# Kernel tuning notes

Measured on AMD Instinct MI355X. Metric: run time of the kernel, lower is better.

Reference implementation:

```python
import jax, jax.numpy as jnp
import numpy as np

B, N1, N2, D, H, DFF = 128, 256, 256, 256, 8, 1024
DH = D // H


def _ln(x, g, b, eps=1e-6):
    mu = jnp.mean(x, axis=-1, keepdims=True)
    var = jnp.mean(jnp.square(x - mu), axis=-1, keepdims=True)
    return g * (x - mu) / jnp.sqrt(var + eps) + b


def setup_inputs() -> dict:
    key = jax.random.key(0)
    ks = jax.random.split(key, 16)
    x1 = jax.random.normal(ks[0], (B, N1, D), jnp.float32)
    x2 = jax.random.normal(ks[1], (B, N2, D), jnp.float32)
    adj1 = (jax.random.uniform(ks[2], (B, N1, N1)) < 0.1).astype(jnp.float32)
    adj1 = jnp.maximum(adj1, jnp.eye(N1, dtype=jnp.float32)[None])
    mask1 = jnp.ones((B, N1), jnp.float32)
    mask2 = jnp.ones((B, N2), jnp.float32)
    s = 0.02
    Wq = jax.random.normal(ks[3], (D, D), jnp.float32) * s
    Wk = jax.random.normal(ks[4], (D, D), jnp.float32) * s
    Wv = jax.random.normal(ks[5], (D, D), jnp.float32) * s
    Wo = jax.random.normal(ks[6], (D, D), jnp.float32) * s
    W1 = jax.random.normal(ks[7], (D, DFF), jnp.float32) * s
    W2 = jax.random.normal(ks[8], (DFF, D), jnp.float32) * s
    return {
        "x1": x1, "adj1": adj1, "mask1": mask1, "x2": x2, "mask2": mask2,
        "Wq": Wq, "bq": jnp.zeros((D,), jnp.float32),
        "Wk": Wk, "bk": jnp.zeros((D,), jnp.float32),
        "Wv": Wv, "bv": jnp.zeros((D,), jnp.float32),
        "Wo": Wo, "bo": jnp.zeros((D,), jnp.float32),
        "W1": W1, "b1": jnp.zeros((DFF,), jnp.float32),
        "W2": W2, "b2": jnp.zeros((D,), jnp.float32),
        "g1": jnp.ones((D,), jnp.float32), "be1": jnp.zeros((D,), jnp.float32),
        "g2": jnp.ones((D,), jnp.float32), "be2": jnp.zeros((D,), jnp.float32),
    }


def reference(x1, adj1, mask1, x2, mask2, Wq, bq, Wk, bk, Wv, bv, Wo, bo,
              W1, b1, W2, b2, g1, be1, g2, be2):
    # Multi-head graph attention: self-attention on x1 masked by adjacency,
    # plus cross-attention from x1 to x2 masked by mask2 (PrismGATLayer).
    q = (x1 @ Wq + bq).reshape(B, N1, H, DH)
    k1 = (x1 @ Wk + bk).reshape(B, N1, H, DH)
    v1 = (x1 @ Wv + bv).reshape(B, N1, H, DH)
    k2 = (x2 @ Wk + bk).reshape(B, N2, H, DH)
    v2 = (x2 @ Wv + bv).reshape(B, N2, H, DH)
    scale = 1.0 / jnp.sqrt(jnp.float32(DH))

    s1 = jnp.einsum('bqhd,bkhd->bhqk', q, k1) * scale            # [B,H,N1,N1]
    m1 = adj1[:, None, :, :] * mask1[:, None, None, :]
    s1 = jnp.where(m1 > 0, s1, jnp.float32(-1e9))
    c1 = jnp.einsum('bhqk,bkhd->bqhd', jax.nn.softmax(s1, axis=-1), v1)

    s2 = jnp.einsum('bqhd,bkhd->bhqk', q, k2) * scale            # [B,H,N1,N2]
    s2 = jnp.where(mask2[:, None, None, :] > 0, s2, jnp.float32(-1e9))
    c2 = jnp.einsum('bhqk,bkhd->bqhd', jax.nn.softmax(s2, axis=-1), v2)

    attn = (c1 + c2).reshape(B, N1, D) @ Wo + bo
    out1 = _ln(x1 + attn, g1, be1)                               # dropout = identity (eval)
    ffn = jax.nn.relu(out1 @ W1 + b1) @ W2 + b2
    return _ln(out1 + ffn, g2, be2)
```

## Files before the change

kernel.cpp:

```cpp
#include <hip/hip_runtime.h>
#include <hip/hip_bf16.h>
#include <stdint.h>

#define B_   128
#define N1_  256
#define N2_  256
#define D_   256
#define H_   8
#define DH_  32
#define DFF_ 1024
#define M_   (B_*N1_)

typedef unsigned short ushortT;
typedef unsigned int   uintT;
typedef short bf16x8 __attribute__((ext_vector_type(8)));
typedef float f32x4  __attribute__((ext_vector_type(4)));

#if __has_builtin(__builtin_amdgcn_exp2f)
#define EXP2(x) __builtin_amdgcn_exp2f(x)
#else
#define EXP2(x) exp2f(x)
#endif

__device__ __forceinline__ float b2f(ushortT u){ return __uint_as_float(((uintT)u)<<16); }
__device__ __forceinline__ ushortT f2b(float f){
  uintT u = __float_as_uint(f);
  uintT r = (u + 0x7fffu + ((u>>16)&1u)) >> 16;
  return (ushortT)r;
}

__device__ __forceinline__ int sniff_wave(const ushortT* x){
  const int e = (x[threadIdx.x & 63] >> 7) & 0xff;
  const unsigned long long bad = __ballot(e < 100 || e > 135);
  return __popcll(bad) >= 12;
}
__device__ __forceinline__ float ldin(const void* p, size_t i, int f32){
  return f32 ? ((const float*)p)[i] : b2f(((const ushortT*)p)[i]);
}

__global__ __launch_bounds__(256) void conv_bf16_kernel(
    const void* __restrict__ X, ushortT* __restrict__ Y, int n8,
    const ushortT* __restrict__ sniffp)
{
  const int in_f32 = sniff_wave(sniffp);
  int i = blockIdx.x * 256 + threadIdx.x;
  if (i >= n8) return;
  size_t base = (size_t)i * 8;
  if (in_f32) {
    float4 a = *(const float4*)((const float*)X + base);
    float4 b = *(const float4*)((const float*)X + base + 4);
    ushort4 o0, o1;
    o0.x=f2b(a.x); o0.y=f2b(a.y); o0.z=f2b(a.z); o0.w=f2b(a.w);
    o1.x=f2b(b.x); o1.y=f2b(b.y); o1.z=f2b(b.z); o1.w=f2b(b.w);
    *(ushort4*)(Y + base)     = o0;
    *(ushort4*)(Y + base + 4) = o1;
  } else {
    *(uint4*)(Y + base) = *(const uint4*)((const ushortT*)X + base);
  }
}

__global__ __launch_bounds__(256) void transpose_w_kernel(
    const void* __restrict__ W, ushortT* __restrict__ Wt, int K, int N,
    const ushortT* __restrict__ sniffp)
{
  const int in_f32 = sniff_wave(sniffp);
  __shared__ float t[32][33];
  const int tx = threadIdx.x & 31, ty = threadIdx.x >> 5;
  const int n0 = blockIdx.x * 32, k0 = blockIdx.y * 32;
  #pragma unroll
  for (int i = 0; i < 4; i++)
    t[ty + 8*i][tx] = ldin(W, (size_t)(k0 + ty + 8*i) * N + n0 + tx, in_f32);
  __syncthreads();
  #pragma unroll
  for (int i = 0; i < 4; i++)
    Wt[(size_t)(n0 + ty + 8*i) * K + k0 + tx] = f2b(t[tx][ty + 8*i]);
}

__global__ __launch_bounds__(256) void pack_adj_kernel(
    const void* __restrict__ ADJ, uintT* __restrict__ AB,
    const ushortT* __restrict__ sniffp)
{
  const int in_f32 = sniff_wave(sniffp);
  const int idx = blockIdx.x * 256 + threadIdx.x;
  const size_t base = (size_t)(idx >> 3) * 256 + (size_t)(idx & 7) * 32;
  uintT bits = 0;
  if (in_f32) {
    const float* ap = (const float*)ADJ + base;
    #pragma unroll
    for (int j4 = 0; j4 < 8; j4++) {
      float4 v = *(const float4*)(ap + j4 * 4);
      bits |= (v.x > 0.f ? 1u : 0u) << (j4 * 4 + 0);
      bits |= (v.y > 0.f ? 1u : 0u) << (j4 * 4 + 1);
      bits |= (v.z > 0.f ? 1u : 0u) << (j4 * 4 + 2);
      bits |= (v.w > 0.f ? 1u : 0u) << (j4 * 4 + 3);
    }
  } else {
    const ushortT* ap = (const ushortT*)ADJ + base;
    #pragma unroll
    for (int j = 0; j < 32; j++)
      bits |= (b2f(ap[j]) > 0.f ? 1u : 0u) << j;
  }
  AB[idx] = bits;
}

__global__ __launch_bounds__(256) void pack_mask_kernel(
    const void* __restrict__ M1, const void* __restrict__ M2,
    uintT* __restrict__ MW, const ushortT* __restrict__ sniffp)
{
  const int in_f32 = sniff_wave(sniffp);
  const int idx = blockIdx.x * 256 + threadIdx.x;
  const int src = idx >> 10;
  const void* MP = src ? M2 : M1;
  const size_t base = (size_t)((idx >> 3) & 127) * 256 + (size_t)(idx & 7) * 32;
  uintT bits = 0;
  #pragma unroll
  for (int j = 0; j < 32; j++)
    bits |= (ldin(MP, base + j, in_f32) > 0.f ? 1u : 0u) << j;
  MW[idx] = bits;
}

__global__ __launch_bounds__(256) void gemm128_kernel(
    const ushortT* __restrict__ A, const ushortT* __restrict__ Bt,
    const void* __restrict__ bias, ushortT* __restrict__ C,
    int M, int N, int K, int relu, float alpha,
    const ushortT* __restrict__ sniffp)
{
  __shared__ ushortT Al[128 * 40];
  __shared__ ushortT Bl[128 * 40];

  const int tid = threadIdx.x;
  const int in_f32 = sniff_wave(sniffp);
  const int wave = tid >> 6, lane = tid & 63;
  const int l15 = lane & 15, l4 = lane >> 4;
  const int wm = wave & 1, wn = wave >> 1;

  const int lin = blockIdx.x + gridDim.x * blockIdx.y;
  const int chunk = (gridDim.x * gridDim.y) >> 3;
  const int gsw = (lin & 7) * chunk + (lin >> 3);
  const int ylog = 31 - __clz(gridDim.y);
  const int bx = gsw >> ylog, by = gsw & (gridDim.y - 1);
  const int row0 = bx * 128, col0 = by * 128;
  const int m0 = wm * 64, n0 = wn * 64;

  f32x4 acc[4][4];
  #pragma unroll
  for (int i = 0; i < 4; i++)
    #pragma unroll
    for (int j = 0; j < 4; j++) acc[i][j] = (f32x4)0.f;

  const int sr = tid >> 2;
  const int sk = (tid & 3) * 8;

  const ushortT* Ap = &A[(size_t)(row0 + sr) * K + sk];
  const ushortT* Bp = &Bt[(size_t)(col0 + sr) * K + sk];
  const size_t step64 = (size_t)64 * K;

  uint4 a0 = *(const uint4*)Ap;
  uint4 a1 = *(const uint4*)(Ap + step64);
  uint4 b0 = *(const uint4*)Bp;
  uint4 b1 = *(const uint4*)(Bp + step64);

  for (int kt = 0; kt < K; kt += 32) {
    __syncthreads();
    *(uint4*)&Al[sr * 40 + sk]        = a0;
    *(uint4*)&Al[(sr + 64) * 40 + sk] = a1;
    *(uint4*)&Bl[sr * 40 + sk]        = b0;
    *(uint4*)&Bl[(sr + 64) * 40 + sk] = b1;
    __syncthreads();
    if (kt + 32 < K) {
      a0 = *(const uint4*)(Ap + kt + 32);
      a1 = *(const uint4*)(Ap + step64 + kt + 32);
      b0 = *(const uint4*)(Bp + kt + 32);
      b1 = *(const uint4*)(Bp + step64 + kt + 32);
    }
    bf16x8 af[4], bf[4];
    #pragma unroll
    for (int mt = 0; mt < 4; mt++)
      af[mt] = *(const bf16x8*)&Al[(m0 + mt * 16 + l15) * 40 + l4 * 8];
    #pragma unroll
    for (int nt = 0; nt < 4; nt++)
      bf[nt] = *(const bf16x8*)&Bl[(n0 + nt * 16 + l15) * 40 + l4 * 8];
    #pragma unroll
    for (int mt = 0; mt < 4; mt++)
      #pragma unroll
      for (int nt = 0; nt < 4; nt++)
        acc[mt][nt] = __builtin_amdgcn_mfma_f32_16x16x32_bf16(af[mt], bf[nt], acc[mt][nt], 0, 0, 0);
  }

  #pragma unroll
  for (int nt = 0; nt < 4; nt++) {
    int col = col0 + n0 + nt * 16 + l15;
    float bb = ldin(bias, col, in_f32);
    #pragma unroll
    for (int mt = 0; mt < 4; mt++) {
      #pragma unroll
      for (int r = 0; r < 4; r++) {
        float v = (acc[mt][nt][r] + bb) * alpha;
        if (relu) v = fmaxf(v, 0.f);
        int row = row0 + m0 + mt * 16 + l4 * 4 + r;
        C[(size_t)row * N + col] = f2b(v);
      }
    }
  }
}

__global__ __launch_bounds__(256) void gemm_qkv_kernel(
    const ushortT* __restrict__ A, const ushortT* __restrict__ Bt,
    const void* __restrict__ b0p, const void* __restrict__ b1p,
    const void* __restrict__ b2p,
    ushortT* __restrict__ C0, ushortT* __restrict__ C1,
    ushortT* __restrict__ C2,
    int K, float alpha2, const ushortT* __restrict__ sniffp)
{
  __shared__ ushortT Al[128 * 40];
  __shared__ ushortT Bl[128 * 40];

  const int tid = threadIdx.x;
  const int in_f32 = sniff_wave(sniffp);
  const int wave = tid >> 6, lane = tid & 63;
  const int l15 = lane & 15, l4 = lane >> 4;
  const int wm = wave & 1, wn = wave >> 1;

  const int gy = gridDim.y;
  const int lin = blockIdx.x + gridDim.x * blockIdx.y;
  const int chunk = (gridDim.x * gy) >> 3;
  const int gsw = (lin & 7) * chunk + (lin >> 3);
  const int bx = gsw / gy, by = gsw - bx * gy;
  const int row0 = bx * 128, col0 = by * 128;
  const int m0 = wm * 64, n0 = wn * 64;

  f32x4 acc[4][4];
  #pragma unroll
  for (int i = 0; i < 4; i++)
    #pragma unroll
    for (int j = 0; j < 4; j++) acc[i][j] = (f32x4)0.f;

  const int sr = tid >> 2;
  const int sk = (tid & 3) * 8;

  const ushortT* Ap = &A[(size_t)(row0 + sr) * K + sk];
  const ushortT* Bp = &Bt[(size_t)(col0 + sr) * K + sk];
  const size_t step64 = (size_t)64 * K;

  uint4 a0 = *(const uint4*)Ap;
  uint4 a1 = *(const uint4*)(Ap + step64);
  uint4 b0 = *(const uint4*)Bp;
  uint4 b1 = *(const uint4*)(Bp + step64);

  for (int kt = 0; kt < K; kt += 32) {
    __syncthreads();
    *(uint4*)&Al[sr * 40 + sk]        = a0;
    *(uint4*)&Al[(sr + 64) * 40 + sk] = a1;
    *(uint4*)&Bl[sr * 40 + sk]        = b0;
    *(uint4*)&Bl[(sr + 64) * 40 + sk] = b1;
    __syncthreads();
    if (kt + 32 < K) {
      a0 = *(const uint4*)(Ap + kt + 32);
      a1 = *(const uint4*)(Ap + step64 + kt + 32);
      b0 = *(const uint4*)(Bp + kt + 32);
      b1 = *(const uint4*)(Bp + step64 + kt + 32);
    }
    bf16x8 af[4], bf[4];
    #pragma unroll
    for (int mt = 0; mt < 4; mt++)
      af[mt] = *(const bf16x8*)&Al[(m0 + mt * 16 + l15) * 40 + l4 * 8];
    #pragma unroll
    for (int nt = 0; nt < 4; nt++)
      bf[nt] = *(const bf16x8*)&Bl[(n0 + nt * 16 + l15) * 40 + l4 * 8];
    #pragma unroll
    for (int mt = 0; mt < 4; mt++)
      #pragma unroll
      for (int nt = 0; nt < 4; nt++)
        acc[mt][nt] = __builtin_amdgcn_mfma_f32_16x16x32_bf16(af[mt], bf[nt], acc[mt][nt], 0, 0, 0);
  }

  const int seg = col0 >> 8;
  const int cb  = col0 & 255;

  if (seg == 1) {
    const int bb  = row0 >> 8;
    const int tl0 = (row0 & 255) + m0 + l4 * 4;
    #pragma unroll
    for (int nt = 0; nt < 4; nt++) {
      const int col = cb + n0 + nt * 16 + l15;
      const float bbv = ldin(b1p, col, in_f32);
      #pragma unroll
      for (int mt = 0; mt < 4; mt++) {
        ushort4 o;
        o.x = f2b(acc[mt][nt][0] + bbv);
        o.y = f2b(acc[mt][nt][1] + bbv);
        o.z = f2b(acc[mt][nt][2] + bbv);
        o.w = f2b(acc[mt][nt][3] + bbv);
        *(ushort4*)&C1[(size_t)bb * 65536 + (size_t)col * 256 + tl0 + mt * 16] = o;
      }
    }
  } else {
    ushortT* C = seg ? C2 : C0;
    const void* bp = seg ? b2p : b0p;
    const float al = seg ? alpha2 : 1.f;
    #pragma unroll
    for (int nt = 0; nt < 4; nt++) {
      const int col = cb + n0 + nt * 16 + l15;
      const float bb = ldin(bp, col, in_f32);
      #pragma unroll
      for (int mt = 0; mt < 4; mt++) {
        #pragma unroll
        for (int r = 0; r < 4; r++) {
          const float v = (acc[mt][nt][r] + bb) * al;
          const int row = row0 + m0 + mt * 16 + l4 * 4 + r;
          C[(size_t)row * 256 + col] = f2b(v);
        }
      }
    }
  }
}

#define LNROWS 4
__global__ __launch_bounds__(256) void add_ln_kernel(
    const void* __restrict__ X, const ushortT* __restrict__ Y,
    const void* __restrict__ gamma, const void* __restrict__ beta,
    void* __restrict__ out, const ushortT* __restrict__ sniffp,
    int x_dyn, int store_dyn)
{
  const int in_f32 = sniff_wave(sniffp);
  const int xf32 = x_dyn ? in_f32 : 0;
  const int lane = threadIdx.x & 63;
  const int gw = blockIdx.x * 4 + (threadIdx.x >> 6);
  const int d0 = lane * 4;

  float g[4], be[4];
  if (in_f32) {
    float4 gv = *(const float4*)((const float*)gamma + d0);
    float4 bv = *(const float4*)((const float*)beta  + d0);
    g[0]=gv.x; g[1]=gv.y; g[2]=gv.z; g[3]=gv.w;
    be[0]=bv.x; be[1]=bv.y; be[2]=bv.z; be[3]=bv.w;
  } else {
    ushort4 gv = *(const ushort4*)((const ushortT*)gamma + d0);
    ushort4 bv = *(const ushort4*)((const ushortT*)beta  + d0);
    g[0]=b2f(gv.x); g[1]=b2f(gv.y); g[2]=b2f(gv.z); g[3]=b2f(gv.w);
    be[0]=b2f(bv.x); be[1]=b2f(bv.y); be[2]=b2f(bv.z); be[3]=b2f(bv.w);
  }

  const int row0 = gw * LNROWS;

  float v[LNROWS][4];
  #pragma unroll
  for (int rr = 0; rr < LNROWS; rr++) {
    const size_t base = (size_t)(row0 + rr) * D_ + d0;
    const ushort4 yv = *(const ushort4*)(Y + base);
    if (xf32) {
      float4 xv = *(const float4*)((const float*)X + base);
      v[rr][0] = xv.x + b2f(yv.x); v[rr][1] = xv.y + b2f(yv.y);
      v[rr][2] = xv.z + b2f(yv.z); v[rr][3] = xv.w + b2f(yv.w);
    } else {
      ushort4 xv = *(const ushort4*)((const ushortT*)X + base);
      v[rr][0] = b2f(xv.x) + b2f(yv.x); v[rr][1] = b2f(xv.y) + b2f(yv.y);
      v[rr][2] = b2f(xv.z) + b2f(yv.z); v[rr][3] = b2f(xv.w) + b2f(yv.w);
    }
  }

  #pragma unroll
  for (int rr = 0; rr < LNROWS; rr++) {
    float s = (v[rr][0] + v[rr][1]) + (v[rr][2] + v[rr][3]);
    float q = (v[rr][0]*v[rr][0] + v[rr][1]*v[rr][1])
            + (v[rr][2]*v[rr][2] + v[rr][3]*v[rr][3]);
    #pragma unroll
    for (int off = 1; off < 64; off <<= 1) {
      s += __shfl_xor(s, off, 64);
      q += __shfl_xor(q, off, 64);
    }
    const float mu   = s * (1.f / D_);
    const float var  = q * (1.f / D_) - mu * mu;
    const float rstd = rsqrtf(var + 1e-6f);
    const size_t base = (size_t)(row0 + rr) * D_ + d0;
    if (store_dyn && in_f32) {
      float4 o;
      o.x = g[0]*(v[rr][0]-mu)*rstd + be[0];
      o.y = g[1]*(v[rr][1]-mu)*rstd + be[1];
      o.z = g[2]*(v[rr][2]-mu)*rstd + be[2];
      o.w = g[3]*(v[rr][3]-mu)*rstd + be[3];
      *(float4*)((float*)out + base) = o;
    } else {
      ushort4 o;
      o.x = f2b(g[0]*(v[rr][0]-mu)*rstd + be[0]);
      o.y = f2b(g[1]*(v[rr][1]-mu)*rstd + be[1]);
      o.z = f2b(g[2]*(v[rr][2]-mu)*rstd + be[2]);
      o.w = f2b(g[3]*(v[rr][3]-mu)*rstd + be[3]);
      *(ushort4*)((ushortT*)out + base) = o;
    }
  }
}

__global__ __launch_bounds__(256, 4) void attn_mfma_kernel(
    ushortT* __restrict__ QC,
    const ushortT* __restrict__ K1, const ushortT* __restrict__ K2,
    const ushortT* __restrict__ V1t, const ushortT* __restrict__ V2t,
    const uintT* __restrict__ AB, const uintT* __restrict__ MW)
{
  const int lin = blockIdx.x + (blockIdx.y << 2) + (blockIdx.z << 5);
  const int gsw = (lin & 7) * 512 + (lin >> 3);
  const int b = gsw >> 5, h = (gsw >> 2) & 7, qt = gsw & 3;
  const int q0 = qt * 64;
  const int tid = threadIdx.x;
  const int wave = tid >> 6, lane = tid & 63;
  const int l15 = lane & 15, l4 = lane >> 4;

  __shared__ __align__(16) ushortT P[64][256];

  const size_t bh = (size_t)b * 256;
  const int prow = wave * 16 + l15;
  const uintT swz = (uintT)((prow & 7) << 4);
  char* Prow = (char*)&P[prow][0];

  uintT adjr[8];
  {
    const uintT* abp = AB + ((size_t)(b * 256 + q0 + prow)) * 8;
    const uint4 a0 = *(const uint4*)abp;
    const uint4 a1 = *(const uint4*)(abp + 4);
    adjr[0]=a0.x; adjr[1]=a0.y; adjr[2]=a0.z; adjr[3]=a0.w;
    adjr[4]=a1.x; adjr[5]=a1.y; adjr[6]=a1.z; adjr[7]=a1.w;
  }

  const bf16x8 af = *(const bf16x8*)&QC[(bh + q0 + wave*16 + l15) * 256 + h*32 + l4*8];

  f32x4 acc0 = (f32x4)0.f, acc1 = (f32x4)0.f;

  #pragma unroll 1
  for (int src = 0; src < 2; src++) {
    const ushortT* Kp  = src ? K2  : K1;
    const ushortT* Vtp = src ? V2t : V1t;

    const uintT* mwp = MW + (src * 128 + b) * 8;
    uintT mww[8];
    #pragma unroll
    for (int w = 0; w < 8; w++) mww[w] = mwp[w];

    float rsum = 0.f;
    #pragma unroll
    for (int c = 0; c < 4; c++) {
      bf16x8 kf[4];
      #pragma unroll
      for (int j = 0; j < 4; j++)
        kf[j] = *(const bf16x8*)&Kp[(bh + (c*4 + j)*16 + l15) * 256 + h*32 + l4*8];
      #pragma unroll
      for (int j = 0; j < 4; j++) {
        const int nt = c*4 + j;
        const f32x4 s4 = __builtin_amdgcn_mfma_f32_16x16x32_bf16(kf[j], af, (f32x4)0.f, 0, 0, 0);
        const int tb = nt*16 + l4*4;
        const int sh = tb & 31;
        uintT bits = mww[nt >> 1] >> sh;
        if (src == 0) bits &= adjr[nt >> 1] >> sh;
        const float e0 = (bits & 1u) ? EXP2(s4[0]) : 0.f;
        const float e1 = (bits & 2u) ? EXP2(s4[1]) : 0.f;
        const float e2 = (bits & 4u) ? EXP2(s4[2]) : 0.f;
        const float e3 = (bits & 8u) ? EXP2(s4[3]) : 0.f;
        rsum += (e0 + e1) + (e2 + e3);
        uintT pk01, pk23;
        asm("v_cvt_pk_bf16_f32 %0, %1, %2" : "=v"(pk01) : "v"(e0), "v"(e1));
        asm("v_cvt_pk_bf16_f32 %0, %1, %2" : "=v"(pk23) : "v"(e2), "v"(e3));
        uint2 pw; pw.x = pk01; pw.y = pk23;
        *(uint2*)(Prow + (((uintT)(tb*2)) ^ swz)) = pw;
      }
    }
    rsum += __shfl_xor(rsum, 16, 64);
    rsum += __shfl_xor(rsum, 32, 64);
    const float rv = 1.f / rsum;
    float rvr[4];
    #pragma unroll
    for (int r = 0; r < 4; r++) rvr[r] = __shfl(rv, l4*4 + r, 64);

    f32x4 o0 = (f32x4)0.f, o1 = (f32x4)0.f;
    __builtin_amdgcn_s_setprio(1);
    #pragma unroll
    for (int kt = 0; kt < 8; kt++) {
      const bf16x8 ap = *(const bf16x8*)(Prow + (((uintT)(kt*64 + l4*16)) ^ swz));
      const bf16x8 v0 = *(const bf16x8*)&Vtp[(bh + h*32 + l15) * 256 + kt*32 + l4*8];
      const bf16x8 v1 = *(const bf16x8*)&Vtp[(bh + h*32 + 16 + l15) * 256 + kt*32 + l4*8];
      o0 = __builtin_amdgcn_mfma_f32_16x16x32_bf16(ap, v0, o0, 0, 0, 0);
      o1 = __builtin_amdgcn_mfma_f32_16x16x32_bf16(ap, v1, o1, 0, 0, 0);
    }
    __builtin_amdgcn_s_setprio(0);
    #pragma unroll
    for (int r = 0; r < 4; r++) { acc0[r] += o0[r] * rvr[r]; acc1[r] += o1[r] * rvr[r]; }
  }

  #pragma unroll
  for (int r = 0; r < 4; r++) {
    const int row = (int)(bh + q0 + wave*16 + l4*4 + r);
    QC[(size_t)row * 256 + h*32 + l15]      = f2b(acc0[r]);
    QC[(size_t)row * 256 + h*32 + 16 + l15] = f2b(acc1[r]);
  }
}

extern "C" void kernel_launch(void* const* d_in, const int* in_sizes, int n_in,
                              void* d_out, int out_size, void* d_ws, size_t ws_size,
                              hipStream_t stream) {
  const void* x1    = d_in[0];
  const void* adj1  = d_in[1];
  const void* mask1 = d_in[2];
  const void* x2    = d_in[3];
  const void* mask2 = d_in[4];
  const void* Wq = d_in[5];  const void* bq = d_in[6];
  const void* Wk = d_in[7];  const void* bk = d_in[8];
  const void* Wv = d_in[9];  const void* bv = d_in[10];
  const void* Wo = d_in[11]; const void* bo = d_in[12];
  const void* W1 = d_in[13]; const void* b1 = d_in[14];
  const void* W2 = d_in[15]; const void* b2 = d_in[16];
  const void* g1 = d_in[17]; const void* be1= d_in[18];
  const void* g2 = d_in[19]; const void* be2= d_in[20];
  const ushortT* sniffp = (const ushortT*)x1;

  ushortT* ws = (ushortT*)d_ws;
  const size_t SZ = (size_t)M_ * D_;
  ushortT* S0 = ws;
  ushortT* S1 = ws + SZ;
  ushortT* S2 = ws + 2*SZ;
  ushortT* S3 = ws + 3*SZ;
  ushortT* S4 = ws + 4*SZ;
  ushortT* S5 = ws + 5*SZ;
  ushortT* dOut = (ushortT*)d_out;

  ushortT* Wkt = S5;
  ushortT* Wvt = S5 + 65536;
  ushortT* Wqt = S5 + 131072;
  ushortT* Wot = S2;
  ushortT* W1t = dOut;
  ushortT* W2t = dOut + 262144;
  ushortT* qbuf = dOut + 524288;
  uintT* AB = (uintT*)(dOut + 9437184);
  uintT* MWp = AB + 262144;

  const float qalpha = 0.25503486f;

  dim3 blk(256);
  dim3 gGemmD(M_/128, D_/128);
  dim3 gGemmF(M_/128, DFF_/128);
  dim3 gQKV(M_/128, 6);
  dim3 gKV(M_/128, 4);
  dim3 gT256(8, 8);
  const int n8 = (int)(SZ / 8);

  pack_adj_kernel<<<dim3(1024), blk, 0, stream>>>(adj1, AB, sniffp);
  pack_mask_kernel<<<dim3(8), blk, 0, stream>>>(mask1, mask2, MWp, sniffp);

  conv_bf16_kernel<<<dim3((n8+255)/256), blk, 0, stream>>>(x2, S2, n8, sniffp);
  transpose_w_kernel<<<gT256, blk, 0, stream>>>(Wk, Wkt, D_, D_, sniffp);
  transpose_w_kernel<<<gT256, blk, 0, stream>>>(Wv, Wvt, D_, D_, sniffp);
  transpose_w_kernel<<<gT256, blk, 0, stream>>>(Wq, Wqt, D_, D_, sniffp);

  gemm_qkv_kernel<<<gKV, blk, 0, stream>>>(S2, S5, bk, bv, nullptr,
                                           S3, S1, nullptr, D_, 1.f, sniffp);

  conv_bf16_kernel<<<dim3((n8+255)/256), blk, 0, stream>>>(x1, S0, n8, sniffp);

  gemm_qkv_kernel<<<gQKV, blk, 0, stream>>>(S0, S5, bk, bv, bq,
                                            S2, S4, qbuf, D_, qalpha, sniffp);

  transpose_w_kernel<<<dim3(DFF_/32, D_/32), blk, 0, stream>>>(W1, W1t, D_, DFF_, sniffp);
  transpose_w_kernel<<<dim3(D_/32, DFF_/32), blk, 0, stream>>>(W2, W2t, DFF_, D_, sniffp);

  attn_mfma_kernel<<<dim3(N1_/64, H_, B_), blk, 0, stream>>>(
      qbuf, S2, S3, S4, S1, AB, MWp);

  transpose_w_kernel<<<gT256, blk, 0, stream>>>(Wo, Wot, D_, D_, sniffp);
  gemm128_kernel<<<gGemmD, blk, 0, stream>>>(qbuf, Wot, bo, S3, M_, D_, D_, 0, 1.f, sniffp);

  add_ln_kernel<<<dim3(M_/16), blk, 0, stream>>>(x1, S3, g1, be1, S0, sniffp, 1, 0);

  gemm128_kernel<<<gGemmF, blk, 0, stream>>>(S0, W1t, b1, S1, M_, DFF_, D_, 1, 1.f, sniffp);

  gemm128_kernel<<<gGemmD, blk, 0, stream>>>(S1, W2t, b2, S5, M_, D_, DFF_, 0, 1.f, sniffp);

  add_ln_kernel<<<dim3(M_/16), blk, 0, stream>>>(S0, S5, g2, be2, d_out, sniffp, 0, 1);
}
```

Baseline: 472.0 us.

## Load GEMM tiles directly into LDS with global_load_lds and XOR swizzle

Both GEMM kernels now load A/B tiles straight from global memory into shared memory using the global_load_lds builtin instead of staging through registers. The padded 40-element row stride is replaced by a 32-element stride with an XOR column swizzle on both write and read sides to avoid bank conflicts. This drops register staging and VGPR pressure, but it also removes the register prefetch of the next K tile, so global load latency is no longer overlapped with MFMA work within a block. The correctness of this relies on the load-to-LDS completing before the barrier.

```diff
diff --git a/kernel.cpp b/kernel.cpp
--- a/kernel.cpp
+++ b/kernel.cpp
@@ -21,6 +21,11 @@
 #else
 #define EXP2(x) exp2f(x)
 #endif
+
+#define GLOAD16(gsrc, ldst)                                                  \
+  __builtin_amdgcn_global_load_lds(                                          \
+      (const __attribute__((address_space(1))) unsigned int*)(gsrc),         \
+      (__attribute__((address_space(3))) unsigned int*)(ldst), 16, 0, 0)
 
 __device__ __forceinline__ float b2f(ushortT u){ return __uint_as_float(((uintT)u)<<16); }
 __device__ __forceinline__ ushortT f2b(float f){
@@ -125,8 +130,8 @@
     int M, int N, int K, int relu, float alpha,
     const ushortT* __restrict__ sniffp)
 {
-  __shared__ ushortT Al[128 * 40];
-  __shared__ ushortT Bl[128 * 40];
+  __shared__ ushortT Al[128 * 32];
+  __shared__ ushortT Bl[128 * 32];
 
   const int tid = threadIdx.x;
   const int in_f32 = sniff_wave(sniffp);
@@ -149,37 +154,31 @@
     for (int j = 0; j < 4; j++) acc[i][j] = (f32x4)0.f;
 
   const int sr = tid >> 2;
-  const int sk = (tid & 3) * 8;
-
-  const ushortT* Ap = &A[(size_t)(row0 + sr) * K + sk];
-  const ushortT* Bp = &Bt[(size_t)(col0 + sr) * K + sk];
+  const int csw = ((tid & 3) ^ ((sr >> 1) & 3)) * 8;
+  const int rsw = (l4 ^ ((l15 >> 1) & 3)) * 8;
+
+  const ushortT* Ap = &A[(size_t)(row0 + sr) * K + csw];
+  const ushortT* Bp = &Bt[(size_t)(col0 + sr) * K + csw];
   const size_t step64 = (size_t)64 * K;
-
-  uint4 a0 = *(const uint4*)Ap;
-  uint4 a1 = *(const uint4*)(Ap + step64);
-  uint4 b0 = *(const uint4*)Bp;
-  uint4 b1 = *(const uint4*)(Bp + step64);
+  ushortT* Ald0 = &Al[tid * 8];
+  ushortT* Ald1 = &Al[2048 + tid * 8];
+  ushortT* Bld0 = &Bl[tid * 8];
+  ushortT* Bld1 = &Bl[2048 + tid * 8];
 
   for (int kt = 0; kt < K; kt += 32) {
     __syncthreads();
-    *(uint4*)&Al[sr * 40 + sk]        = a0;
-    *(uint4*)&Al[(sr + 64) * 40 + sk] = a1;
-    *(uint4*)&Bl[sr * 40 + sk]        = b0;
-    *(uint4*)&Bl[(sr + 64) * 40 + sk] = b1;
+    GLOAD16(Ap + kt,          Ald0);
+    GLOAD16(Ap + step64 + kt, Ald1);
+    GLOAD16(Bp + kt,          Bld0);
+    GLOAD16(Bp + step64 + kt, Bld1);
     __syncthreads();
-    if (kt + 32 < K) {
-      a0 = *(const uint4*)(Ap + kt + 32);
-      a1 = *(const uint4*)(Ap + step64 + kt + 32);
-      b0 = *(const uint4*)(Bp + kt + 32);
-      b1 = *(const uint4*)(Bp + step64 + kt + 32);
-    }
     bf16x8 af[4], bf[4];
     #pragma unroll
     for (int mt = 0; mt < 4; mt++)
-      af[mt] = *(const bf16x8*)&Al[(m0 + mt * 16 + l15) * 40 + l4 * 8];
+      af[mt] = *(const bf16x8*)&Al[(m0 + mt * 16 + l15) * 32 + rsw];
     #pragma unroll
     for (int nt = 0; nt < 4; nt++)
-      bf[nt] = *(const bf16x8*)&Bl[(n0 + nt * 16 + l15) * 40 + l4 * 8];
+      bf[nt] = *(const bf16x8*)&Bl[(n0 + nt * 16 + l15) * 32 + rsw];
     #pragma unroll
     for (int mt = 0; mt < 4; mt++)
       #pragma unroll
@@ -212,8 +211,8 @@
     ushortT* __restrict__ C2,
     int K, float alpha2, const ushortT* __restrict__ sniffp)
 {
-  __shared__ ushortT Al[128 * 40];
-  __shared__ ushortT Bl[128 * 40];
+  __shared__ ushortT Al[128 * 32];
+  __shared__ ushortT Bl[128 * 32];
 
   const int tid = threadIdx.x;
   const int in_f32 = sniff_wave(sniffp);
@@ -236,37 +235,31 @@
     for (int j = 0; j < 4; j++) acc[i][j] = (f32x4)0.f;
 
   const int sr = tid >> 2;
-  const int sk = (tid & 3) * 8;
-
-  const ushortT* Ap = &A[(size_t)(row0 + sr) * K + sk];
-  const ushortT* Bp = &Bt[(size_t)(col0 + sr) * K + sk];
+  const int csw = ((tid & 3) ^ ((sr >> 1) & 3)) * 8;
+  const int rsw = (l4 ^ ((l15 >> 1) & 3)) * 8;
+
+  const ushortT* Ap = &A[(size_t)(row0 + sr) * K + csw];
+  const ushortT* Bp = &Bt[(size_t)(col0 + sr) * K + csw];
   const size_t step64 = (size_t)64 * K;
-
-  uint4 a0 = *(const uint4*)Ap;
-  uint4 a1 = *(const uint4*)(Ap + step64);
-  uint4 b0 = *(const uint4*)Bp;
-  uint4 b1 = *(const uint4*)(Bp + step64);
+  ushortT* Ald0 = &Al[tid * 8];
+  ushortT* Ald1 = &Al[2048 + tid * 8];
+  ushortT* Bld0 = &Bl[tid * 8];
+  ushortT* Bld1 = &Bl[2048 + tid * 8];
 
   for (int kt = 0; kt < K; kt += 32) {
     __syncthreads();
-    *(uint4*)&Al[sr * 40 + sk]        = a0;
-    *(uint4*)&Al[(sr + 64) * 40 + sk] = a1;
-    *(uint4*)&Bl[sr * 40 + sk]        = b0;
-    *(uint4*)&Bl[(sr + 64) * 40 + sk] = b1;
+    GLOAD16(Ap + kt,          Ald0);
+    GLOAD16(Ap + step64 + kt, Ald1);
+    GLOAD16(Bp + kt,          Bld0);
+    GLOAD16(Bp + step64 + kt, Bld1);
     __syncthreads();
-    if (kt + 32 < K) {
-      a0 = *(const uint4*)(Ap + kt + 32);
-      a1 = *(const uint4*)(Ap + step64 + kt + 32);
-      b0 = *(const uint4*)(Bp + kt + 32);
-      b1 = *(const uint4*)(Bp + step64 + kt + 32);
-    }
     bf16x8 af[4], bf[4];
     #pragma unroll
     for (int mt = 0; mt < 4; mt++)
-      af[mt] = *(const bf16x8*)&Al[(m0 + mt * 16 + l15) * 40 + l4 * 8];
+      af[mt] = *(const bf16x8*)&Al[(m0 + mt * 16 + l15) * 32 + rsw];
     #pragma unroll
     for (int nt = 0; nt < 4; nt++)
-      bf[nt] = *(const bf16x8*)&Bl[(n0 + nt * 16 + l15) * 40 + l4 * 8];
+      bf[nt] = *(const bf16x8*)&Bl[(n0 + nt * 16 + l15) * 32 + rsw];
     #pragma unroll
     for (int mt = 0; mt < 4; mt++)
       #pragma unroll
```

Result: no change. 479.5 us (+1.6%).

## Fuse input conversion into QKV GEMM and merge prep kernels into one launch

Applied to the files above, without the earlier changes.

Drops the separate x1/x2 fp32-to-bf16 conversion kernels; the merged K/V/Q projection GEMM now loads fp32 inputs directly and converts them in registers. The two QKV GEMM launches become one 10-column grid covering both x2 (K,V) and x1 (K,V,Q). All weight transposes and the adjacency and mask bit-packing move into a single prep kernel. This cuts launch count and the round trip of writing and re-reading the bf16 copies of the activations. The cost is more register and ALU work inside the GEMM loads, plus a wider grid.

```diff
diff --git a/kernel.cpp b/kernel.cpp
--- a/kernel.cpp
+++ b/kernel.cpp
@@ -38,35 +38,29 @@
   return f32 ? ((const float*)p)[i] : b2f(((const ushortT*)p)[i]);
 }
 
-__global__ __launch_bounds__(256) void conv_bf16_kernel(
-    const void* __restrict__ X, ushortT* __restrict__ Y, int n8,
-    const ushortT* __restrict__ sniffp)
-{
-  const int in_f32 = sniff_wave(sniffp);
-  int i = blockIdx.x * 256 + threadIdx.x;
-  if (i >= n8) return;
-  size_t base = (size_t)i * 8;
-  if (in_f32) {
-    float4 a = *(const float4*)((const float*)X + base);
-    float4 b = *(const float4*)((const float*)X + base + 4);
-    ushort4 o0, o1;
-    o0.x=f2b(a.x); o0.y=f2b(a.y); o0.z=f2b(a.z); o0.w=f2b(a.w);
-    o1.x=f2b(b.x); o1.y=f2b(b.y); o1.z=f2b(b.z); o1.w=f2b(b.w);
-    *(ushort4*)(Y + base)     = o0;
-    *(ushort4*)(Y + base + 4) = o1;
+template<int F32>
+__device__ __forceinline__ uint4 ldA8(const void* A, size_t e){
+  if (F32) {
+    const float* p = (const float*)A + e;
+    const float4 a = *(const float4*)p;
+    const float4 b = *(const float4*)(p + 4);
+    uint4 r;
+    r.x = (uintT)f2b(a.x) | ((uintT)f2b(a.y) << 16);
+    r.y = (uintT)f2b(a.z) | ((uintT)f2b(a.w) << 16);
+    r.z = (uintT)f2b(b.x) | ((uintT)f2b(b.y) << 16);
+    r.w = (uintT)f2b(b.z) | ((uintT)f2b(b.w) << 16);
+    return r;
   } else {
-    *(uint4*)(Y + base) = *(const uint4*)((const ushortT*)X + base);
-  }
-}
-
-__global__ __launch_bounds__(256) void transpose_w_kernel(
-    const void* __restrict__ W, ushortT* __restrict__ Wt, int K, int N,
-    const ushortT* __restrict__ sniffp)
-{
-  const int in_f32 = sniff_wave(sniffp);
-  __shared__ float t[32][33];
+    return *(const uint4*)((const ushortT*)A + e);
+  }
+}
+
+__device__ __forceinline__ void tw_body(
+    const void* W, ushortT* Wt, int K, int N, int xb, int yb, int in_f32,
+    float (*t)[33])
+{
   const int tx = threadIdx.x & 31, ty = threadIdx.x >> 5;
-  const int n0 = blockIdx.x * 32, k0 = blockIdx.y * 32;
+  const int n0 = xb * 32, k0 = yb * 32;
   #pragma unroll
   for (int i = 0; i < 4; i++)
     t[ty + 8*i][tx] = ldin(W, (size_t)(k0 + ty + 8*i) * N + n0 + tx, in_f32);
@@ -76,47 +70,72 @@
     Wt[(size_t)(n0 + ty + 8*i) * K + k0 + tx] = f2b(t[tx][ty + 8*i]);
 }
 
-__global__ __launch_bounds__(256) void pack_adj_kernel(
+__global__ __launch_bounds__(256) void prep_kernel(
     const void* __restrict__ ADJ, uintT* __restrict__ AB,
+    const void* __restrict__ M1, const void* __restrict__ M2,
+    uintT* __restrict__ MW,
+    const void* __restrict__ Wk, const void* __restrict__ Wv,
+    const void* __restrict__ Wq, const void* __restrict__ Wo,
+    ushortT* __restrict__ Wpack,
+    const void* __restrict__ W1, ushortT* __restrict__ W1t,
+    const void* __restrict__ W2, ushortT* __restrict__ W2t,
     const ushortT* __restrict__ sniffp)
 {
+  __shared__ float t[32][33];
   const int in_f32 = sniff_wave(sniffp);
-  const int idx = blockIdx.x * 256 + threadIdx.x;
-  const size_t base = (size_t)(idx >> 3) * 256 + (size_t)(idx & 7) * 32;
-  uintT bits = 0;
-  if (in_f32) {
-    const float* ap = (const float*)ADJ + base;
-    #pragma unroll
-    for (int j4 = 0; j4 < 8; j4++) {
-      float4 v = *(const float4*)(ap + j4 * 4);
-      bits |= (v.x > 0.f ? 1u : 0u) << (j4 * 4 + 0);
-      bits |= (v.y > 0.f ? 1u : 0u) << (j4 * 4 + 1);
-      bits |= (v.z > 0.f ? 1u : 0u) << (j4 * 4 + 2);
-      bits |= (v.w > 0.f ? 1u : 0u) << (j4 * 4 + 3);
-    }
-  } else {
-    const ushortT* ap = (const ushortT*)ADJ + base;
+  const int bid = blockIdx.x;
+
+  if (bid < 1024) {
+    const int idx = bid * 256 + threadIdx.x;
+    const size_t base = (size_t)(idx >> 3) * 256 + (size_t)(idx & 7) * 32;
+    uintT bits = 0;
+    if (in_f32) {
+      const float* ap = (const float*)ADJ + base;
+      #pragma unroll
+      for (int j4 = 0; j4 < 8; j4++) {
+        float4 v = *(const float4*)(ap + j4 * 4);
+        bits |= (v.x > 0.f ? 1u : 0u) << (j4 * 4 + 0);
+        bits |= (v.y > 0.f ? 1u : 0u) << (j4 * 4 + 1);
+        bits |= (v.z > 0.f ? 1u : 0u) << (j4 * 4 + 2);
+        bits |= (v.w > 0.f ? 1u : 0u) << (j4 * 4 + 3);
+      }
+    } else {
+      const ushortT* ap = (const ushortT*)ADJ + base;
+      #pragma unroll
+      for (int j = 0; j < 32; j++)
+        bits |= (b2f(ap[j]) > 0.f ? 1u : 0u) << j;
+    }
+    AB[idx] = bits;
+    return;
+  }
+  if (bid < 1032) {
+    const int idx = (bid - 1024) * 256 + threadIdx.x;
+    const int src = idx >> 10;
+    const void* MP = src ? M2 : M1;
+    const size_t base = (size_t)((idx >> 3) & 127) * 256 + (size_t)(idx & 7) * 32;
+    uintT bits = 0;
     #pragma unroll
     for (int j = 0; j < 32; j++)
-      bits |= (b2f(ap[j]) > 0.f ? 1u : 0u) << j;
-  }
-  AB[idx] = bits;
-}
-
-__global__ __launch_bounds__(256) void pack_mask_kernel(
-    const void* __restrict__ M1, const void* __restrict__ M2,
-    uintT* __restrict__ MW, const ushortT* __restrict__ sniffp)
-{
-  const int in_f32 = sniff_wave(sniffp);
-  const int idx = blockIdx.x * 256 + threadIdx.x;
-  const int src = idx >> 10;
-  const void* MP = src ? M2 : M1;
-  const size_t base = (size_t)((idx >> 3) & 127) * 256 + (size_t)(idx & 7) * 32;
-  uintT bits = 0;
-  #pragma unroll
-  for (int j = 0; j < 32; j++)
-    bits |= (ldin(MP, base + j, in_f32) > 0.f ? 1u : 0u) << j;
-  MW[idx] = bits;
+      bits |= (ldin(MP, base + j, in_f32) > 0.f ? 1u : 0u) << j;
+    MW[idx] = bits;
+    return;
+  }
+  if (bid < 1288) {
+    const int idx = bid - 1032;
+    const int z = idx >> 6, yb = (idx >> 3) & 7, xb = idx & 7;
+    const void* W = (z == 0) ? Wk : (z == 1) ? Wv : (z == 2) ? Wq : Wo;
+    tw_body(W, Wpack + (size_t)z * 65536, 256, 256, xb, yb, in_f32, t);
+    return;
+  }
+  if (bid < 1544) {
+    const int idx = bid - 1288;
+    tw_body(W1, W1t, 256, 1024, idx & 31, idx >> 5, in_f32, t);
+    return;
+  }
+  {
+    const int idx = bid - 1544;
+    tw_body(W2, W2t, 1024, 256, idx & 7, idx >> 3, in_f32, t);
+  }
 }
 
 __global__ __launch_bounds__(256) void gemm128_kernel(
@@ -204,29 +223,30 @@
   }
 }
 
-__global__ __launch_bounds__(256) void gemm_qkv_kernel(
-    const ushortT* __restrict__ A, const ushortT* __restrict__ Bt,
-    const void* __restrict__ b0p, const void* __restrict__ b1p,
-    const void* __restrict__ b2p,
-    ushortT* __restrict__ C0, ushortT* __restrict__ C1,
-    ushortT* __restrict__ C2,
-    int K, float alpha2, const ushortT* __restrict__ sniffp)
-{
-  __shared__ ushortT Al[128 * 40];
-  __shared__ ushortT Bl[128 * 40];
-
+template<int F32>
+__device__ __forceinline__ void kvqkv_body(
+    const void* __restrict__ X2, const void* __restrict__ X1,
+    const ushortT* __restrict__ Wt,
+    const void* __restrict__ bk, const void* __restrict__ bv,
+    const void* __restrict__ bq,
+    ushortT* __restrict__ K2o, ushortT* __restrict__ V2to,
+    ushortT* __restrict__ K1o, ushortT* __restrict__ V1to,
+    ushortT* __restrict__ Qo, float qalpha,
+    ushortT* Al, ushortT* Bl)
+{
   const int tid = threadIdx.x;
-  const int in_f32 = sniff_wave(sniffp);
   const int wave = tid >> 6, lane = tid & 63;
   const int l15 = lane & 15, l4 = lane >> 4;
   const int wm = wave & 1, wn = wave >> 1;
 
-  const int gy = gridDim.y;
-  const int lin = blockIdx.x + gridDim.x * blockIdx.y;
-  const int chunk = (gridDim.x * gy) >> 3;
-  const int gsw = (lin & 7) * chunk + (lin >> 3);
-  const int bx = gsw / gy, by = gsw - bx * gy;
-  const int row0 = bx * 128, col0 = by * 128;
+  const int lin = blockIdx.x + 256 * blockIdx.y;
+  const int gsw = (lin & 7) * 320 + (lin >> 3);
+  const int bx = gsw / 10, by = gsw - bx * 10;
+  const int row0 = bx * 128;
+  const int grp = by >= 4;
+  const int lby = grp ? by - 4 : by;
+  const void* A = grp ? X1 : X2;
+  const int brow0 = lby * 128;
   const int m0 = wm * 64, n0 = wn * 64;
 
   f32x4 acc[4][4];
@@ -238,27 +258,26 @@
   const int sr = tid >> 2;
   const int sk = (tid & 3) * 8;
 
-  const ushortT* Ap = &A[(size_t)(row0 + sr) * K + sk];
-  const ushortT* Bp = &Bt[(size_t)(col0 + sr) * K + sk];
-  const size_t step64 = (size_t)64 * K;
-
-  uint4 a0 = *(const uint4*)Ap;
-  uint4 a1 = *(const uint4*)(Ap + step64);
+  const size_t aBase = (size_t)(row0 + sr) * 256 + sk;
+  const ushortT* Bp = &Wt[(size_t)(brow0 + sr) * 256 + sk];
+
+  uint4 a0 = ldA8<F32>(A, aBase);
+  uint4 a1 = ldA8<F32>(A, aBase + 64 * 256);
   uint4 b0 = *(const uint4*)Bp;
-  uint4 b1 = *(const uint4*)(Bp + step64);
-
-  for (int kt = 0; kt < K; kt += 32) {
+  uint4 b1 = *(const uint4*)(Bp + 64 * 256);
+
+  for (int kt = 0; kt < 256; kt += 32) {
     __syncthreads();
     *(uint4*)&Al[sr * 40 + sk]        = a0;
     *(uint4*)&Al[(sr + 64) * 40 + sk] = a1;
     *(uint4*)&Bl[sr * 40 + sk]        = b0;
     *(uint4*)&Bl[(sr + 64) * 40 + sk] = b1;
     __syncthreads();
-    if (kt + 32 < K) {
-      a0 = *(const uint4*)(Ap + kt + 32);
-      a1 = *(const uint4*)(Ap + step64 + kt + 32);
+    if (kt + 32 < 256) {
+      a0 = ldA8<F32>(A, aBase + kt + 32);
+      a1 = ldA8<F32>(A, aBase + 64 * 256 + kt + 32);
       b0 = *(const uint4*)(Bp + kt + 32);
-      b1 = *(const uint4*)(Bp + step64 + kt + 32);
+      b1 = *(const uint4*)(Bp + 64 * 256 + kt + 32);
     }
     bf16x8 af[4], bf[4];
     #pragma unroll
@@ -274,16 +293,17 @@
         acc[mt][nt] = __builtin_amdgcn_mfma_f32_16x16x32_bf16(af[mt], bf[nt], acc[mt][nt], 0, 0, 0);
   }
 
-  const int seg = col0 >> 8;
-  const int cb  = col0 & 255;
+  const int seg = lby >> 1;
+  const int cb  = (lby & 1) * 128;
 
   if (seg == 1) {
+    ushortT* Vt = grp ? V1to : V2to;
     const int bb  = row0 >> 8;
     const int tl0 = (row0 & 255) + m0 + l4 * 4;
     #pragma unroll
     for (int nt = 0; nt < 4; nt++) {
       const int col = cb + n0 + nt * 16 + l15;
-      const float bbv = ldin(b1p, col, in_f32);
+      const float bbv = ldin(bv, col, F32);
       #pragma unroll
       for (int mt = 0; mt < 4; mt++) {
         ushort4 o;
@@ -291,17 +311,17 @@
         o.y = f2b(acc[mt][nt][1] + bbv);
         o.z = f2b(acc[mt][nt][2] + bbv);
         o.w = f2b(acc[mt][nt][3] + bbv);
-        *(ushort4*)&C1[(size_t)bb * 65536 + (size_t)col * 256 + tl0 + mt * 16] = o;
+        *(ushort4*)&Vt[(size_t)bb * 65536 + (size_t)col * 256 + tl0 + mt * 16] = o;
       }
     }
   } else {
-    ushortT* C = seg ? C2 : C0;
-    const void* bp = seg ? b2p : b0p;
-    const float al = seg ? alpha2 : 1.f;
+    ushortT* C = (seg == 2) ? Qo : (grp ? K1o : K2o);
+    const void* bp = (seg == 2) ? bq : bk;
+    const float al = (seg == 2) ? qalpha : 1.f;
     #pragma unroll
     for (int nt = 0; nt < 4; nt++) {
       const int col = cb + n0 + nt * 16 + l15;
-      const float bb = ldin(bp, col, in_f32);
+      const float bb = ldin(bp, col, F32);
       #pragma unroll
       for (int mt = 0; mt < 4; mt++) {
         #pragma unroll
@@ -313,6 +333,25 @@
       }
     }
   }
+}
+
+__global__ __launch_bounds__(256) void gemm_kvqkv_kernel(
+    const void* __restrict__ X2, const void* __restrict__ X1,
+    const ushortT* __restrict__ Wt,
+    const void* __restrict__ bk, const void* __restrict__ bv,
+    const void* __restrict__ bq,
+    ushortT* __restrict__ K2o, ushortT* __restrict__ V2to,
+    ushortT* __restrict__ K1o, ushortT* __restrict__ V1to,
+    ushortT* __restrict__ Qo, float qalpha,
+    const ushortT* __restrict__ sniffp)
+{
+  __shared__ ushortT Al[128 * 40];
+  __shared__ ushortT Bl[128 * 40];
+  const int in_f32 = sniff_wave(sniffp);
+  if (in_f32)
+    kvqkv_body<1>(X2, X1, Wt, bk, bv, bq, K2o, V2to, K1o, V1to, Qo, qalpha, Al, Bl);
+  else
+    kvqkv_body<0>(X2, X1, Wt, bk, bv, bq, K2o, V2to, K1o, V1to, Qo, qalpha, Al, Bl);
 }
 
 #define LNROWS 4
@@ -520,10 +559,8 @@
   ushortT* S5 = ws + 5*SZ;
   ushortT* dOut = (ushortT*)d_out;
 
-  ushortT* Wkt = S5;
-  ushortT* Wvt = S5 + 65536;
-  ushortT* Wqt = S5 + 131072;
-  ushortT* Wot = S2;
+  ushortT* Wpack = S5;
+  ushortT* Wot   = S5 + 196608;
   ushortT* W1t = dOut;
   ushortT* W2t = dOut + 262144;
   ushortT* qbuf = dOut + 524288;
@@ -535,34 +572,17 @@
   dim3 blk(256);
   dim3 gGemmD(M_/128, D_/128);
   dim3 gGemmF(M_/128, DFF_/128);
-  dim3 gQKV(M_/128, 6);
-  dim3 gKV(M_/128, 4);
-  dim3 gT256(8, 8);
-  const int n8 = (int)(SZ / 8);
-
-  pack_adj_kernel<<<dim3(1024), blk, 0, stream>>>(adj1, AB, sniffp);
-  pack_mask_kernel<<<dim3(8), blk, 0, stream>>>(mask1, mask2, MWp, sniffp);
-
-  conv_bf16_kernel<<<dim3((n8+255)/256), blk, 0, stream>>>(x2, S2, n8, sniffp);
-  transpose_w_kernel<<<gT256, blk, 0, stream>>>(Wk, Wkt, D_, D_, sniffp);
-  transpose_w_kernel<<<gT256, blk, 0, stream>>>(Wv, Wvt, D_, D_, sniffp);
-  transpose_w_kernel<<<gT256, blk, 0, stream>>>(Wq, Wqt, D_, D_, sniffp);
-
-  gemm_qkv_kernel<<<gKV, blk, 0, stream>>>(S2, S5, bk, bv, nullptr,
-                                           S3, S1, nullptr, D_, 1.f, sniffp);
-
-  conv_bf16_kernel<<<dim3((n8+255)/256), blk, 0, stream>>>(x1, S0, n8, sniffp);
-
-  gemm_qkv_kernel<<<gQKV, blk, 0, stream>>>(S0, S5, bk, bv, bq,
-                                            S2, S4, qbuf, D_, qalpha, sniffp);
-
-  transpose_w_kernel<<<dim3(DFF_/32, D_/32), blk, 0, stream>>>(W1, W1t, D_, DFF_, sniffp);
-  transpose_w_kernel<<<dim3(D_/32, DFF_/32), blk, 0, stream>>>(W2, W2t, DFF_, D_, sniffp);
+  dim3 gKVQKV(256, 10);
+
+  prep_kernel<<<dim3(1800), blk, 0, stream>>>(
+      adj1, AB, mask1, mask2, MWp, Wk, Wv, Wq, Wo, Wpack, W1, W1t, W2, W2t, sniffp);
+
+  gemm_kvqkv_kernel<<<gKVQKV, blk, 0, stream>>>(
+      x2, x1, Wpack, bk, bv, bq, S3, S1, S2, S4, qbuf, qalpha, sniffp);
 
   attn_mfma_kernel<<<dim3(N1_/64, H_, B_), blk, 0, stream>>>(
       qbuf, S2, S3, S4, S1, AB, MWp);
 
-  transpose_w_kernel<<<gT256, blk, 0, stream>>>(Wo, Wot, D_, D_, sniffp);
   gemm128_kernel<<<gGemmD, blk, 0, stream>>>(qbuf, Wot, bo, S3, M_, D_, D_, 0, 1.f, sniffp);
 
   add_ln_kernel<<<dim3(M_/16), blk, 0, stream>>>(x1, S3, g1, be1, S0, sniffp, 1, 0);
```

After: 452.8 us. 4.1% less time.
